# Performance work log

Hardware: AMD Instinct MI355X
Metric: run time of the kernel (lower is better)

Reference implementation:

```python
import jax, jax.numpy as jnp
import numpy as np

GH, GW, H, B, IN = 4, 2, 512, 8192, 1
FC_HID = H // 2
NC = GH * GW
BN_EPS = 1e-5


def setup_inputs() -> dict:
    key = jax.random.key(0)
    ks = jax.random.split(key, 20)
    def n(k, shape, s=1.0):
        return jax.random.normal(k, shape, dtype=jnp.float32) * s
    return {
        "x": n(ks[0], (B, GH, GW)),
        "h_ext": n(ks[1], (B, H), 0.1),
        "c_ext": n(ks[2], (B, H), 0.1),
        "grid_h": n(ks[3], (GH, GW, B, H), 0.1),
        "grid_c": n(ks[4], (GH, GW, B, H), 0.1),
        "Wh": n(ks[5], (NC, H, 3 * H), (3 * H) ** -0.5),
        "bh": n(ks[6], (NC, H), 0.01),
        "Wc": n(ks[7], (NC, H, 3 * H), (3 * H) ** -0.5),
        "bc": n(ks[8], (NC, H), 0.01),
        "W_ih": n(ks[9], (NC, 4 * H, IN), 1.0),
        "W_hh": n(ks[10], (NC, 4 * H, H), H ** -0.5),
        "b_ih": n(ks[11], (NC, 4 * H), 0.01),
        "b_hh": n(ks[12], (NC, 4 * H), 0.01),
        "W1": n(ks[13], (FC_HID, 2 * H), (2 * H) ** -0.5),
        "b1": n(ks[14], (FC_HID,), 0.01),
        "W2": n(ks[15], (1, FC_HID), FC_HID ** -0.5),
        "b2": n(ks[16], (1,), 0.01),
        "gamma": jnp.ones((1,), jnp.float32),
        "beta": jnp.zeros((1,), jnp.float32),
    }


def _lattice_forward(x, h_ext, c_ext, grid_h, grid_c, Wh, bh, Wc, bc,
                     W_ih, W_hh, b_ih, b_hh, W1, b1, W2, b2, gamma, beta):
    b = x.shape[0]
    zeros = jnp.zeros((b, H), x.dtype)
    # python lists over the small fixed 4x2 grid (strict left/up dependency)
    sh = [[grid_h[i, j] for j in range(GW)] for i in range(GH)]
    sc = [[grid_c[i, j] for j in range(GW)] for i in range(GH)]
    for i in range(GH):
        for j in range(GW):
            k = i * GW + j
            h_prev, c_prev = sh[i][j], sc[i][j]
            if i == 0 and j == 0:
                h_left, c_left = h_ext, c_ext
            elif j > 0:
                h_left, c_left = sh[i][j - 1], sc[i][j - 1]
            else:
                h_left, c_left = zeros, zeros
            if i > 0:
                h_up, c_up = sh[i - 1][j], sc[i - 1][j]
            else:
                h_up, c_up = zeros, zeros
            comb_h = jnp.concatenate([h_left, h_up, h_prev], axis=1)  # [B,3H]
            comb_c = jnp.concatenate([c_left, c_up, c_prev], axis=1)
            ph = comb_h @ Wh[k].T + bh[k]  # [B,H]
            pc = comb_c @ Wc[k].T + bc[k]
            xi = x[:, i, j][:, None]  # [B,1]
            gates = xi @ W_ih[k].T + b_ih[k] + ph @ W_hh[k].T + b_hh[k]  # [B,4H]
            ig, fg, gg, og = jnp.split(gates, 4, axis=1)
            c_new = jax.nn.sigmoid(fg) * pc + jax.nn.sigmoid(ig) * jnp.tanh(gg)
            h_new = jax.nn.sigmoid(og) * jnp.tanh(c_new)
            sh[i][j], sc[i][j] = h_new, c_new
    final_h = sh[-1][-1] + h_ext
    final_c = sc[-1][-1] + c_ext
    final = jnp.concatenate([final_h, final_c], axis=1)  # [B,2H]
    hid = jax.nn.relu(final @ W1.T + b1)
    out = hid @ W2.T + b2  # [B,1]
    # BatchNorm1d in training mode: biased batch stats over the batch dim
    mu = jnp.mean(out, axis=0, keepdims=True)
    var = jnp.mean((out - mu) ** 2, axis=0, keepdims=True)
    out = gamma * (out - mu) * jax.lax.rsqrt(var + BN_EPS) + beta
    out = jax.nn.sigmoid(out)
    new_gh = jnp.stack([jnp.stack(row) for row in sh])  # [GH,GW,B,H]
    new_gc = jnp.stack([jnp.stack(row) for row in sc])
    return out, final_h, final_c, new_gh, new_gc


def reference(x, h_ext, c_ext, grid_h, grid_c, Wh, bh, Wc, bc,
              W_ih, W_hh, b_ih, b_hh, W1, b1, W2, b2, gamma, beta):
    return _lattice_forward(x, h_ext, c_ext, grid_h, grid_c, Wh, bh, Wc, bc,
                            W_ih, W_hh, b_ih, b_hh, W1, b1, W2, b2, gamma, beta)
```

## Files before the change

kernel.cpp:

```cpp
#include <hip/hip_runtime.h>
#include <stdint.h>

#define B_SZ 8192
static const size_t BH = (size_t)B_SZ * 512;

typedef short bfrag8 __attribute__((ext_vector_type(8)));
typedef float f32x4 __attribute__((ext_vector_type(4)));

__device__ __forceinline__ unsigned short f2bf(float f) {
  union { float f; uint32_t u; } c; c.f = f;
  uint32_t u = c.u;
  uint32_t r = (u + 0x7FFFu + ((u >> 16) & 1u)) >> 16;
  return (unsigned short)r;
}
__device__ __forceinline__ float bf2f(unsigned short u) {
  union { uint32_t u; float f; } c; c.u = ((uint32_t)u) << 16;
  return c.f;
}
__device__ __forceinline__ uint32_t pk2(float a, float b) {
  uint32_t r;
  asm("v_cvt_pk_bf16_f32 %0, %1, %2" : "=v"(r) : "v"(a), "v"(b));
  return r;
}
__device__ __forceinline__ float sigm(float x) { return 1.0f / (1.0f + __expf(-x)); }
__device__ __forceinline__ float tanh_fast(float x) {
  float cx = fminf(fmaxf(x, -15.0f), 15.0f);
  float e = __expf(2.0f * cx);
  return (e - 1.0f) / (e + 1.0f);
}

__device__ __forceinline__ void gload16(const void* g, void* l) {
  __builtin_amdgcn_global_load_lds(
      (const __attribute__((address_space(1))) void*)g,
      (__attribute__((address_space(3))) void*)l, 16, 0, 0);
}

__device__ __forceinline__ void xcd_swizzle(int& bx, int& by, int& bz) {
  int nx = gridDim.x, ny = gridDim.y, nz = gridDim.z;
  int nwg = nx * ny * nz;
  int id = blockIdx.x + nx * (blockIdx.y + ny * blockIdx.z);
  int q = nwg >> 3, r = nwg & 7;
  int xcd = id & 7, lin = id >> 3;
  int swz = (xcd < r ? xcd * (q + 1) : r * (q + 1) + (xcd - r) * q) + lin;
  bx = swz % nx; swz /= nx;
  by = swz % ny; bz = swz / ny;
}

struct PJob {
  const void* A[3];
  int co[3];
  int nseg, relu;
  const unsigned short* B;
  const float* bias;
  unsigned short* outBf;
};
struct PArgs {
  PJob j[8];
  int ldA, ldB, outStride;
};

template <int AF32>
__global__ __launch_bounds__(256, 4) void pgemm_k(PArgs pa) {
  __shared__ __align__(16) char As[16384];
  __shared__ __align__(16) char Bs[16384];
  int bx, by, bz;
  xcd_swizzle(bx, by, bz);
  const PJob jb = pa.j[bz];
  const int tid = threadIdx.x;
  const int lane = tid & 63;
  const int wv = tid >> 6;
  const int wr = wv >> 1, wc = wv & 1;
  const int m0 = by * 128;
  const int ldA = pa.ldA;

  int rowA[4], cg[4];
  const char* browPtr[4];
#pragma unroll
  for (int q = 0; q < 4; ++q) {
    int cl = q * 256 + tid;
    int row = cl >> 3, cs = cl & 7;
    cg[q] = cs ^ (row & 7);
    rowA[q] = row;
    browPtr[q] = (const char*)jb.B + (size_t)(bx * 128 + row) * pa.ldB * 2;
  }

  f32x4 acc[4][4];
#pragma unroll
  for (int a = 0; a < 4; ++a)
#pragma unroll
    for (int b = 0; b < 4; ++b) acc[a][b] = f32x4{0.f, 0.f, 0.f, 0.f};

  for (int s = 0; s < jb.nseg; ++s) {
    const int coB = jb.co[s] * 2;
    for (int k0 = 0; k0 < 512; k0 += 64) {
#pragma unroll
      for (int q = 0; q < 4; ++q)
        gload16(browPtr[q] + coB + k0 * 2 + cg[q] * 16,
                Bs + (q * 256 + tid) * 16);
      if (AF32) {
        const float* Ab = (const float*)jb.A[s];
#pragma unroll
        for (int q = 0; q < 4; ++q) {
          const float4* p = (const float4*)(Ab + (size_t)(m0 + rowA[q]) * ldA +
                                            k0 + cg[q] * 8);
          float4 a0 = p[0];
          float4 a1 = p[1];
          uint4 w;
          w.x = pk2(a0.x, a0.y);
          w.y = pk2(a0.z, a0.w);
          w.z = pk2(a1.x, a1.y);
          w.w = pk2(a1.z, a1.w);
          *(uint4*)(As + (q * 256 + tid) * 16) = w;
        }
      } else {
        const char* Ab = (const char*)jb.A[s];
#pragma unroll
        for (int q = 0; q < 4; ++q)
          gload16(Ab + ((size_t)(m0 + rowA[q]) * ldA + k0) * 2 + cg[q] * 16,
                  As + (q * 256 + tid) * 16);
      }
      __syncthreads();
#pragma unroll
      for (int ks = 0; ks < 2; ++ks) {
        bfrag8 af[4], bfr[4];
#pragma unroll
        for (int mf = 0; mf < 4; ++mf) {
          int row = wr * 64 + mf * 16 + (lane & 15);
          af[mf] = *(const bfrag8*)(As + row * 128 +
                                    ((ks * 4 + (lane >> 4)) ^ (row & 7)) * 16);
        }
#pragma unroll
        for (int nf = 0; nf < 4; ++nf) {
          int row = wc * 64 + nf * 16 + (lane & 15);
          bfr[nf] = *(const bfrag8*)(Bs + row * 128 +
                                     ((ks * 4 + (lane >> 4)) ^ (row & 7)) * 16);
        }
#pragma unroll
        for (int mf = 0; mf < 4; ++mf)
#pragma unroll
          for (int nf = 0; nf < 4; ++nf)
            acc[mf][nf] = __builtin_amdgcn_mfma_f32_16x16x32_bf16(
                af[mf], bfr[nf], acc[mf][nf], 0, 0, 0);
      }
      __syncthreads();
    }
  }

  const int c4 = lane & 15;
  const int r4 = lane >> 4;
  const int n0 = bx * 128;
#pragma unroll
  for (int nf = 0; nf < 4; ++nf) {
    int colg = n0 + wc * 64 + nf * 16 + c4;
    float bv = jb.bias[colg];
#pragma unroll
    for (int mf = 0; mf < 4; ++mf)
#pragma unroll
      for (int r = 0; r < 4; ++r) {
        int rowg = m0 + wr * 64 + mf * 16 + r4 * 4 + r;
        size_t o = (size_t)rowg * pa.outStride + colg;
        float v = acc[mf][nf][r] + bv;
        if (jb.relu) v = fmaxf(v, 0.0f);
        jb.outBf[o] = f2bf(v);
      }
  }
}

struct GJob {
  const unsigned short* ph;
  const unsigned short* Whh;
  const unsigned short* pc;
  float* gh; float* gc;
  int cell, last;
};
struct GArgs {
  GJob j[2];
  const float* x;
  const float* W_ih; const float* b_ih; const float* b_hh;
  const float* h_ext; const float* c_ext;
  float* fh; float* fc;
  unsigned short* finalB;
};

__global__ __launch_bounds__(512, 2) void gates_k(GArgs ga) {
  extern __shared__ char lds[];
  int bx, by, bz;
  xcd_swizzle(bx, by, bz);
  const GJob jb = ga.j[bz];
  const int tid = threadIdx.x;
  const int lane = tid & 63;
  const int wv = tid >> 6;
  const int wr = wv >> 2;
  const int wc = wv & 3;
  const int m0 = by * 256;

  int rowS[4], cgS[4];
  const char* bPtr[4];
#pragma unroll
  for (int q = 0; q < 4; ++q) {
    int cl = q * 512 + tid;
    int row = cl >> 3, cs = cl & 7;
    cgS[q] = cs ^ (row & 7);
    rowS[q] = row;
    int browG = ((row >> 4) & 3) * 512 + bx * 64 + ((row >> 6) << 4) + (row & 15);
    bPtr[q] = (const char*)jb.Whh + (size_t)browG * 512 * 2;
  }

  auto stage = [&](int t, int buf) {
    int k0 = t << 6;
    char* Ab = lds + buf * 32768;
    char* Bb = lds + 65536 + buf * 32768;
#pragma unroll
    for (int q = 0; q < 4; ++q)
      gload16((const char*)jb.ph + ((size_t)(m0 + rowS[q]) * 512 + k0) * 2 + cgS[q] * 16,
              Ab + (q * 512 + tid) * 16);
#pragma unroll
    for (int q = 0; q < 4; ++q)
      gload16(bPtr[q] + k0 * 2 + cgS[q] * 16, Bb + (q * 512 + tid) * 16);
  };

  f32x4 acc[8][4];
#pragma unroll
  for (int a = 0; a < 8; ++a)
#pragma unroll
    for (int b = 0; b < 4; ++b) acc[a][b] = f32x4{0.f, 0.f, 0.f, 0.f};

  stage(0, 0);
  asm volatile("s_waitcnt vmcnt(0)" ::: "memory");
  __builtin_amdgcn_s_barrier();
  asm volatile("" ::: "memory");

  int cur = 0;
  for (int t = 0; t < 8; ++t) {
    if (t + 1 < 8) stage(t + 1, cur ^ 1);
    const char* As = lds + cur * 32768;
    const char* Bs = lds + 65536 + cur * 32768;
    bfrag8 bfr[4][2];
#pragma unroll
    for (int nf = 0; nf < 4; ++nf)
#pragma unroll
      for (int ks = 0; ks < 2; ++ks) {
        int row = wc * 64 + nf * 16 + (lane & 15);
        bfr[nf][ks] = *(const bfrag8*)(Bs + row * 128 +
                                       (((ks * 4 + (lane >> 4)) ^ (row & 7)) * 16));
      }
#pragma unroll
    for (int mf = 0; mf < 8; ++mf) {
      bfrag8 af[2];
#pragma unroll
      for (int ks = 0; ks < 2; ++ks) {
        int row = wr * 128 + mf * 16 + (lane & 15);
        af[ks] = *(const bfrag8*)(As + row * 128 +
                                  (((ks * 4 + (lane >> 4)) ^ (row & 7)) * 16));
      }
#pragma unroll
      for (int nf = 0; nf < 4; ++nf)
#pragma unroll
        for (int ks = 0; ks < 2; ++ks)
          acc[mf][nf] = __builtin_amdgcn_mfma_f32_16x16x32_bf16(
              af[ks], bfr[nf][ks], acc[mf][nf], 0, 0, 0);
    }
    asm volatile("s_waitcnt vmcnt(0)" ::: "memory");
    __builtin_amdgcn_s_barrier();
    asm volatile("" ::: "memory");
    cur ^= 1;
  }

  const int c4 = lane & 15;
  const int r4 = lane >> 4;
  int hcol = bx * 64 + wc * 16 + c4;
  const float* Wih = ga.W_ih + jb.cell * 2048;
  const float* bih = ga.b_ih + jb.cell * 2048;
  const float* bhh = ga.b_hh + jb.cell * 2048;
  float wih[4], gb[4];
#pragma unroll
  for (int q = 0; q < 4; ++q) {
    wih[q] = Wih[q * 512 + hcol];
    gb[q] = bih[q * 512 + hcol] + bhh[q * 512 + hcol];
  }
#pragma unroll
  for (int mf = 0; mf < 8; ++mf)
#pragma unroll
    for (int r = 0; r < 4; ++r) {
      int b = m0 + wr * 128 + mf * 16 + r4 * 4 + r;
      float xi = ga.x[b * 8 + jb.cell];
      float vi = acc[mf][0][r] + xi * wih[0] + gb[0];
      float vf = acc[mf][1][r] + xi * wih[1] + gb[1];
      float vg = acc[mf][2][r] + xi * wih[2] + gb[2];
      float vo = acc[mf][3][r] + xi * wih[3] + gb[3];
      size_t o = (size_t)b * 512 + hcol;
      float pcv = bf2f(jb.pc[o]);
      float cn = sigm(vf) * pcv + sigm(vi) * tanh_fast(vg);
      float hn = sigm(vo) * tanh_fast(cn);
      jb.gh[o] = hn;
      jb.gc[o] = cn;
      if (jb.last) {
        float fh = hn + ga.h_ext[o];
        float fc = cn + ga.c_ext[o];
        ga.fh[o] = fh;
        ga.fc[o] = fc;
        ga.finalB[(size_t)b * 1024 + hcol] = f2bf(fh);
        ga.finalB[(size_t)b * 1024 + 512 + hcol] = f2bf(fc);
      }
    }
}

struct CvtArgs {
  const float4* s[8];
  uint2* d[8];
  long start[9];
};
__global__ __launch_bounds__(256) void convert_many(CvtArgs ca) {
  long total = ca.start[8];
  long stride = (long)gridDim.x * blockDim.x;
  for (long idx = (long)blockIdx.x * blockDim.x + threadIdx.x; idx < total;
       idx += stride) {
    int jb = 0;
#pragma unroll
    for (int q = 1; q < 8; ++q) jb += (idx >= ca.start[q]) ? 1 : 0;
    long local = idx - ca.start[jb];
    float4 v = ca.s[jb][local];
    uint2 o;
    o.x = (uint32_t)f2bf(v.x) | ((uint32_t)f2bf(v.y) << 16);
    o.y = (uint32_t)f2bf(v.z) | ((uint32_t)f2bf(v.w) << 16);
    ca.d[jb][local] = o;
  }
}

__global__ __launch_bounds__(256)
void fc2_kernel(const unsigned short* hid, const float* W2, const float* b2,
                float* outlin) {
  int row = blockIdx.x * 4 + (threadIdx.x >> 6);
  int lane = threadIdx.x & 63;
  uint2 hv = ((const uint2*)(hid + (size_t)row * 256))[lane];
  float4 wv = ((const float4*)W2)[lane];
  float s = bf2f((unsigned short)(hv.x & 0xffffu)) * wv.x +
            bf2f((unsigned short)(hv.x >> 16)) * wv.y +
            bf2f((unsigned short)(hv.y & 0xffffu)) * wv.z +
            bf2f((unsigned short)(hv.y >> 16)) * wv.w;
#pragma unroll
  for (int o = 32; o > 0; o >>= 1) s += __shfl_down(s, o);
  if (lane == 0) outlin[row] = s + b2[0];
}

__global__ __launch_bounds__(1024)
void bn_kernel(const float* outlin, const float* gamma, const float* beta,
               float* out) {
  __shared__ float sred[16], sred2[16];
  __shared__ float smu, srs;
  float s = 0.f, s2 = 0.f;
  for (int i = threadIdx.x; i < 8192; i += 1024) {
    float v = outlin[i];
    s += v; s2 += v * v;
  }
#pragma unroll
  for (int o = 32; o > 0; o >>= 1) { s += __shfl_down(s, o); s2 += __shfl_down(s2, o); }
  if ((threadIdx.x & 63) == 0) { sred[threadIdx.x >> 6] = s; sred2[threadIdx.x >> 6] = s2; }
  __syncthreads();
  if (threadIdx.x == 0) {
    float S = 0.f, S2 = 0.f;
    for (int q = 0; q < 16; ++q) { S += sred[q]; S2 += sred2[q]; }
    float mu = S * (1.0f / 8192.0f);
    float var = S2 * (1.0f / 8192.0f) - mu * mu;
    smu = mu; srs = rsqrtf(var + 1e-5f);
  }
  __syncthreads();
  float gm = gamma[0], bt = beta[0];
  for (int i = threadIdx.x; i < 8192; i += 1024) {
    float v = (outlin[i] - smu) * srs * gm + bt;
    out[i] = sigm(v);
  }
}

extern "C" void kernel_launch(void* const* d_in, const int* in_sizes, int n_in,
                              void* d_out, int out_size, void* d_ws, size_t ws_size,
                              hipStream_t stream) {
  const float* x      = (const float*)d_in[0];
  const float* h_ext  = (const float*)d_in[1];
  const float* c_ext  = (const float*)d_in[2];
  const float* grid_h = (const float*)d_in[3];
  const float* grid_c = (const float*)d_in[4];
  const float* Wh     = (const float*)d_in[5];
  const float* bh     = (const float*)d_in[6];
  const float* Wc     = (const float*)d_in[7];
  const float* bc     = (const float*)d_in[8];
  const float* W_ih   = (const float*)d_in[9];
  const float* W_hh   = (const float*)d_in[10];
  const float* b_ih   = (const float*)d_in[11];
  const float* b_hh   = (const float*)d_in[12];
  const float* W1     = (const float*)d_in[13];
  const float* b1     = (const float*)d_in[14];
  const float* W2     = (const float*)d_in[15];
  const float* b2     = (const float*)d_in[16];
  const float* gamma  = (const float*)d_in[17];
  const float* beta   = (const float*)d_in[18];

  float* out = (float*)d_out;
  float* fh_out = out + 8192;
  float* fc_out = fh_out + BH;
  float* gh_out = fc_out + BH;
  float* gc_out = gh_out + 8 * BH;

  char* ws = (char*)d_ws;
  size_t off = 0;
  auto alloc = [&](size_t bytes) {
    char* p = ws + off;
    off = (off + bytes + 255) & ~(size_t)255;
    return p;
  };
  unsigned short* whB   = (unsigned short*)alloc(8ull * 512 * 1536 * 2);
  unsigned short* wcB   = (unsigned short*)alloc(8ull * 512 * 1536 * 2);
  unsigned short* whhB  = (unsigned short*)alloc(8ull * 2048 * 512 * 2);
  unsigned short* w1B   = (unsigned short*)alloc(256ull * 1024 * 2);
  unsigned short* pcB   = (unsigned short*)alloc(8 * BH * 2);
  unsigned short* phB   = (unsigned short*)alloc(8 * BH * 2);
  unsigned short* finalB = (unsigned short*)alloc((size_t)B_SZ * 1024 * 2);
  unsigned short* hidB   = (unsigned short*)alloc((size_t)B_SZ * 256 * 2);
  float*          outlin = (float*)alloc((size_t)B_SZ * 4);

  hipFuncSetAttribute((const void*)gates_k,
                      hipFuncAttributeMaxDynamicSharedMemorySize, 131072);

  {
    CvtArgs ca;
    long n4[4] = {8L * 512 * 1536 / 4, 8L * 512 * 1536 / 4,
                  8L * 2048 * 512 / 4, 256L * 1024 / 4};
    const float* srcs[4] = {Wh, Wc, W_hh, W1};
    unsigned short* dsts[4] = {whB, wcB, whhB, w1B};
    ca.start[0] = 0;
    for (int q = 0; q < 8; ++q) {
      int qq = q < 4 ? q : 3;
      ca.s[q] = (const float4*)srcs[qq];
      ca.d[q] = (uint2*)dsts[qq];
      ca.start[q + 1] = ca.start[q] + (q < 4 ? n4[q] : 0);
    }
    convert_many<<<2048, 256, 0, stream>>>(ca);
  }

  auto launch_p = [&](const int* cells, int n) {
    PArgs pa = {};
    pa.ldA = 512; pa.ldB = 1536; pa.outStride = 512;
    for (int q = 0; q < n; ++q) {
      int k = cells[q];
      int i = k >> 1, jj = k & 1;
      PJob& jh = pa.j[2 * q];
      PJob& jc = pa.j[2 * q + 1];
      jh = PJob{}; jc = PJob{};
      int ns = 0;
      if (k == 0) {
        jh.A[ns] = h_ext; jc.A[ns] = c_ext;
        jh.co[ns] = 0; jc.co[ns] = 0; ns++;
      } else if (jj > 0) {
        jh.A[ns] = gh_out + (size_t)(k - 1) * BH;
        jc.A[ns] = gc_out + (size_t)(k - 1) * BH;
        jh.co[ns] = 0; jc.co[ns] = 0; ns++;
      }
      if (i > 0) {
        jh.A[ns] = gh_out + (size_t)(k - 2) * BH;
        jc.A[ns] = gc_out + (size_t)(k - 2) * BH;
        jh.co[ns] = 512; jc.co[ns] = 512; ns++;
      }
      jh.A[ns] = grid_h + (size_t)k * BH;
      jc.A[ns] = grid_c + (size_t)k * BH;
      jh.co[ns] = 1024; jc.co[ns] = 1024; ns++;
      jh.nseg = ns; jc.nseg = ns;
      jh.B = whB + (size_t)k * 512 * 1536; jh.bias = bh + k * 512;
      jc.B = wcB + (size_t)k * 512 * 1536; jc.bias = bc + k * 512;
      jh.outBf = phB + (size_t)k * BH;
      jc.outBf = pcB + (size_t)k * BH;
    }
    pgemm_k<1><<<dim3(4, 64, 2 * n), 256, 0, stream>>>(pa);
  };

  auto launch_gates = [&](const int* cells, int n) {
    GArgs ga = {};
    ga.x = x; ga.W_ih = W_ih; ga.b_ih = b_ih; ga.b_hh = b_hh;
    ga.h_ext = h_ext; ga.c_ext = c_ext;
    ga.fh = fh_out; ga.fc = fc_out; ga.finalB = finalB;
    for (int q = 0; q < n; ++q) {
      int k = cells[q];
      GJob& j = ga.j[q];
      j.ph = phB + (size_t)k * BH;
      j.Whh = whhB + (size_t)k * 2048 * 512;
      j.pc = pcB + (size_t)k * BH;
      j.gh = gh_out + (size_t)k * BH;
      j.gc = gc_out + (size_t)k * BH;
      j.cell = k; j.last = (k == 7);
    }
    gates_k<<<dim3(8, 32, n), 512, 131072, stream>>>(ga);
  };

  const int diags[5][2] = {{0, -1}, {1, 2}, {3, 4}, {5, 6}, {7, -1}};
  const int dn[5] = {1, 2, 2, 2, 1};
  for (int d = 0; d < 5; ++d) {
    launch_p(diags[d], dn[d]);
    launch_gates(diags[d], dn[d]);
  }

  {
    PArgs pa = {};
    pa.ldA = 1024; pa.ldB = 1024; pa.outStride = 256;
    PJob& j = pa.j[0];
    j = PJob{};
    j.A[0] = finalB; j.co[0] = 0;
    j.A[1] = finalB + 512; j.co[1] = 512;
    j.nseg = 2; j.relu = 1;
    j.B = w1B; j.bias = b1; j.outBf = hidB;
    pgemm_k<0><<<dim3(2, 64, 1), 256, 0, stream>>>(pa);
  }

  fc2_kernel<<<2048, 256, 0, stream>>>(hidB, W2, b2, outlin);
  bn_kernel<<<1, 1024, 0, stream>>>(outlin, gamma, beta, out);
}
```

Measured before the change: 732.9 us.

## Use 256x256 double-buffered GEMM tile kernel for lattice projection GEMMs

Replaces the 128x128 single-buffered projection GEMM with a new 256x256-tile, 512-thread kernel that double-buffers A and B in 128KB dynamic LDS. The next tile's fp32 A loads and B global-to-LDS copies are issued before the MFMAs on the current tile, and the bf16 conversion of A is written afterwards. The larger tile cuts global reloads per output and hides load latency. In exchange occupancy drops to one block per CU, fewer blocks launch per diagonal, and register pressure rises with 32 accumulators. The old kernel is kept, without its fp32 path, for the FC1 GEMM.

New measurement: 663.6 us. 9.5% less time.

```diff
diff --git a/kernel.cpp b/kernel.cpp
--- a/kernel.cpp
+++ b/kernel.cpp
@@ -46,122 +46,142 @@
   by = swz % ny; bz = swz / ny;
 }
 
-struct PJob {
-  const void* A[3];
+struct P8Job {
+  const float* A[3];
   int co[3];
-  int nseg, relu;
+  int nseg;
   const unsigned short* B;
   const float* bias;
   unsigned short* outBf;
 };
-struct PArgs {
-  PJob j[8];
-  int ldA, ldB, outStride;
+struct P8Args {
+  P8Job j[4];
+  int ldB, outStride;
 };
 
-template <int AF32>
-__global__ __launch_bounds__(256, 4) void pgemm_k(PArgs pa) {
-  __shared__ __align__(16) char As[16384];
-  __shared__ __align__(16) char Bs[16384];
+__global__ __launch_bounds__(512, 1) void pgemm256_k(P8Args pa) {
+  extern __shared__ char lds[];
   int bx, by, bz;
   xcd_swizzle(bx, by, bz);
-  const PJob jb = pa.j[bz];
+  const P8Job jb = pa.j[bz];
   const int tid = threadIdx.x;
   const int lane = tid & 63;
   const int wv = tid >> 6;
-  const int wr = wv >> 1, wc = wv & 1;
-  const int m0 = by * 128;
-  const int ldA = pa.ldA;
-
-  int rowA[4], cg[4];
-  const char* browPtr[4];
+  const int wr = wv >> 2, wc = wv & 3;
+  const int m0 = by * 256;
+
+  int rowS[4], cgS[4];
+  const char* bPtr[4];
 #pragma unroll
   for (int q = 0; q < 4; ++q) {
-    int cl = q * 256 + tid;
+    int cl = q * 512 + tid;
     int row = cl >> 3, cs = cl & 7;
-    cg[q] = cs ^ (row & 7);
-    rowA[q] = row;
-    browPtr[q] = (const char*)jb.B + (size_t)(bx * 128 + row) * pa.ldB * 2;
-  }
-
-  f32x4 acc[4][4];
-#pragma unroll
-  for (int a = 0; a < 4; ++a)
+    cgS[q] = cs ^ (row & 7);
+    rowS[q] = row;
+    bPtr[q] = (const char*)jb.B + (size_t)(bx * 256 + row) * pa.ldB * 2;
+  }
+
+  auto loadA = [&](int t, float4* a0, float4* a1) {
+    int seg = t >> 3, k0 = (t & 7) << 6;
+    const float* Ab = jb.A[seg];
+#pragma unroll
+    for (int q = 0; q < 4; ++q) {
+      const float4* p = (const float4*)(Ab + (size_t)(m0 + rowS[q]) * 512 + k0 +
+                                        cgS[q] * 8);
+      a0[q] = p[0];
+      a1[q] = p[1];
+    }
+  };
+  auto stageB = [&](int t, int buf) {
+    int seg = t >> 3, k0 = (t & 7) << 6;
+    int coB = (jb.co[seg] + k0) * 2;
+    char* Bb = lds + 65536 + buf * 32768;
+#pragma unroll
+    for (int q = 0; q < 4; ++q)
+      gload16(bPtr[q] + coB + cgS[q] * 16, Bb + (q * 512 + tid) * 16);
+  };
+  auto writeA = [&](const float4* a0, const float4* a1, int buf) {
+    char* Ab = lds + buf * 32768;
+#pragma unroll
+    for (int q = 0; q < 4; ++q) {
+      uint4 w;
+      w.x = pk2(a0[q].x, a0[q].y);
+      w.y = pk2(a0[q].z, a0[q].w);
+      w.z = pk2(a1[q].x, a1[q].y);
+      w.w = pk2(a1[q].z, a1[q].w);
+      *(uint4*)(Ab + (q * 512 + tid) * 16) = w;
+    }
+  };
+
+  f32x4 acc[8][4];
+#pragma unroll
+  for (int a = 0; a < 8; ++a)
 #pragma unroll
     for (int b = 0; b < 4; ++b) acc[a][b] = f32x4{0.f, 0.f, 0.f, 0.f};
 
-  for (int s = 0; s < jb.nseg; ++s) {
-    const int coB = jb.co[s] * 2;
-    for (int k0 = 0; k0 < 512; k0 += 64) {
-#pragma unroll
-      for (int q = 0; q < 4; ++q)
-        gload16(browPtr[q] + coB + k0 * 2 + cg[q] * 16,
-                Bs + (q * 256 + tid) * 16);
-      if (AF32) {
-        const float* Ab = (const float*)jb.A[s];
-#pragma unroll
-        for (int q = 0; q < 4; ++q) {
-          const float4* p = (const float4*)(Ab + (size_t)(m0 + rowA[q]) * ldA +
-                                            k0 + cg[q] * 8);
-          float4 a0 = p[0];
-          float4 a1 = p[1];
-          uint4 w;
-          w.x = pk2(a0.x, a0.y);
-          w.y = pk2(a0.z, a0.w);
-          w.z = pk2(a1.x, a1.y);
-          w.w = pk2(a1.z, a1.w);
-          *(uint4*)(As + (q * 256 + tid) * 16) = w;
-        }
-      } else {
-        const char* Ab = (const char*)jb.A[s];
-#pragma unroll
-        for (int q = 0; q < 4; ++q)
-          gload16(Ab + ((size_t)(m0 + rowA[q]) * ldA + k0) * 2 + cg[q] * 16,
-                  As + (q * 256 + tid) * 16);
-      }
-      __syncthreads();
+  const int nt = jb.nseg * 8;
+
+  {
+    float4 a0[4], a1[4];
+    loadA(0, a0, a1);
+    stageB(0, 0);
+    writeA(a0, a1, 0);
+  }
+  __syncthreads();
+
+  int cur = 0;
+  for (int t = 0; t < nt; ++t) {
+    float4 a0[4], a1[4];
+    const bool more = (t + 1 < nt);
+    if (more) {
+      loadA(t + 1, a0, a1);
+      stageB(t + 1, cur ^ 1);
+    }
+    const char* As = lds + cur * 32768;
+    const char* Bs = lds + 65536 + cur * 32768;
+    bfrag8 bfr[4][2];
+#pragma unroll
+    for (int nf = 0; nf < 4; ++nf)
 #pragma unroll
       for (int ks = 0; ks < 2; ++ks) {
-        bfrag8 af[4], bfr[4];
-#pragma unroll
-        for (int mf = 0; mf < 4; ++mf) {
-          int row = wr * 64 + mf * 16 + (lane & 15);
-          af[mf] = *(const bfrag8*)(As + row * 128 +
-                                    ((ks * 4 + (lane >> 4)) ^ (row & 7)) * 16);
-        }
-#pragma unroll
-        for (int nf = 0; nf < 4; ++nf) {
-          int row = wc * 64 + nf * 16 + (lane & 15);
-          bfr[nf] = *(const bfrag8*)(Bs + row * 128 +
-                                     ((ks * 4 + (lane >> 4)) ^ (row & 7)) * 16);
-        }
-#pragma unroll
-        for (int mf = 0; mf < 4; ++mf)
-#pragma unroll
-          for (int nf = 0; nf < 4; ++nf)
-            acc[mf][nf] = __builtin_amdgcn_mfma_f32_16x16x32_bf16(
-                af[mf], bfr[nf], acc[mf][nf], 0, 0, 0);
-      }
-      __syncthreads();
-    }
+        int row = wc * 64 + nf * 16 + (lane & 15);
+        bfr[nf][ks] = *(const bfrag8*)(Bs + row * 128 +
+                                       (((ks * 4 + (lane >> 4)) ^ (row & 7)) * 16));
+      }
+#pragma unroll
+    for (int mf = 0; mf < 8; ++mf) {
+      bfrag8 af[2];
+#pragma unroll
+      for (int ks = 0; ks < 2; ++ks) {
+        int row = wr * 128 + mf * 16 + (lane & 15);
+        af[ks] = *(const bfrag8*)(As + row * 128 +
+                                  (((ks * 4 + (lane >> 4)) ^ (row & 7)) * 16));
+      }
+#pragma unroll
+      for (int nf = 0; nf < 4; ++nf)
+#pragma unroll
+        for (int ks = 0; ks < 2; ++ks)
+          acc[mf][nf] = __builtin_amdgcn_mfma_f32_16x16x32_bf16(
+              af[ks], bfr[nf][ks], acc[mf][nf], 0, 0, 0);
+    }
+    if (more) writeA(a0, a1, cur ^ 1);
+    __syncthreads();
+    cur ^= 1;
   }
 
   const int c4 = lane & 15;
   const int r4 = lane >> 4;
-  const int n0 = bx * 128;
+  const int n0 = bx * 256;
 #pragma unroll
   for (int nf = 0; nf < 4; ++nf) {
     int colg = n0 + wc * 64 + nf * 16 + c4;
     float bv = jb.bias[colg];
 #pragma unroll
-    for (int mf = 0; mf < 4; ++mf)
+    for (int mf = 0; mf < 8; ++mf)
 #pragma unroll
       for (int r = 0; r < 4; ++r) {
-        int rowg = m0 + wr * 64 + mf * 16 + r4 * 4 + r;
-        size_t o = (size_t)rowg * pa.outStride + colg;
-        float v = acc[mf][nf][r] + bv;
-        if (jb.relu) v = fmaxf(v, 0.0f);
-        jb.outBf[o] = f2bf(v);
+        int rowg = m0 + wr * 128 + mf * 16 + r4 * 4 + r;
+        jb.outBf[(size_t)rowg * pa.outStride + colg] = f2bf(acc[mf][nf][r] + bv);
       }
   }
 }
@@ -303,6 +323,107 @@
         ga.finalB[(size_t)b * 1024 + 512 + hcol] = f2bf(fc);
       }
     }
+}
+
+struct PJob {
+  const void* A[3];
+  int co[3];
+  int nseg, relu;
+  const unsigned short* B;
+  const float* bias;
+  unsigned short* outBf;
+};
+struct PArgs {
+  PJob j[8];
+  int ldA, ldB, outStride;
+};
+
+__global__ __launch_bounds__(256, 4) void pgemm_k(PArgs pa) {
+  __shared__ __align__(16) char As[16384];
+  __shared__ __align__(16) char Bs[16384];
+  int bx, by, bz;
+  xcd_swizzle(bx, by, bz);
+  const PJob jb = pa.j[bz];
+  const int tid = threadIdx.x;
+  const int lane = tid & 63;
+  const int wv = tid >> 6;
+  const int wr = wv >> 1, wc = wv & 1;
+  const int m0 = by * 128;
+
+  int rowA[4], cg[4];
+  const char* browPtr[4];
+#pragma unroll
+  for (int q = 0; q < 4; ++q) {
+    int cl = q * 256 + tid;
+    int row = cl >> 3, cs = cl & 7;
+    cg[q] = cs ^ (row & 7);
+    rowA[q] = row;
+    browPtr[q] = (const char*)jb.B + (size_t)(bx * 128 + row) * pa.ldB * 2;
+  }
+
+  f32x4 acc[4][4];
+#pragma unroll
+  for (int a = 0; a < 4; ++a)
+#pragma unroll
+    for (int b = 0; b < 4; ++b) acc[a][b] = f32x4{0.f, 0.f, 0.f, 0.f};
+
+  for (int s = 0; s < jb.nseg; ++s) {
+    const char* Abase = (const char*)jb.A[s];
+    const int coB = jb.co[s] * 2;
+    for (int k0 = 0; k0 < 512; k0 += 64) {
+#pragma unroll
+      for (int q = 0; q < 4; ++q)
+        gload16(Abase + ((size_t)(m0 + rowA[q]) * pa.ldA + k0) * 2 + cg[q] * 16,
+                As + (q * 256 + tid) * 16);
+#pragma unroll
+      for (int q = 0; q < 4; ++q)
+        gload16(browPtr[q] + coB + k0 * 2 + cg[q] * 16,
+                Bs + (q * 256 + tid) * 16);
+      __syncthreads();
+#pragma unroll
+      for (int ks = 0; ks < 2; ++ks) {
+        bfrag8 af[4], bfr[4];
+#pragma unroll
+        for (int mf = 0; mf < 4; ++mf) {
+          int row = wr * 64 + mf * 16 + (lane & 15);
+          af[mf] = *(const bfrag8*)(As + row * 128 +
+                                    ((ks * 4 + (lane >> 4)) ^ (row & 7)) * 16);
+        }
+#pragma unroll
+        for (int nf = 0; nf < 4; ++nf) {
+          int row = wc * 64 + nf * 16 + (lane & 15);
+          bfr[nf] = *(const bfrag8*)(Bs + row * 128 +
+                                     ((ks * 4 + (lane >> 4)) ^ (row & 7)) * 16);
+        }
+#pragma unroll
+        for (int mf = 0; mf < 4; ++mf)
+#pragma unroll
+          for (int nf = 0; nf < 4; ++nf)
+            acc[mf][nf] = __builtin_amdgcn_mfma_f32_16x16x32_bf16(
+                af[mf], bfr[nf], acc[mf][nf], 0, 0, 0);
+      }
+      __syncthreads();
+    }
+  }
+
+  const int c4 = lane & 15;
+  const int r4 = lane >> 4;
+  const int n0 = bx * 128;
+#pragma unroll
+  for (int nf = 0; nf < 4; ++nf) {
+    int colg = n0 + wc * 64 + nf * 16 + c4;
+    float bv = jb.bias[colg];
+#pragma unroll
+    for (int mf = 0; mf < 4; ++mf)
+#pragma unroll
+      for (int r = 0; r < 4; ++r) {
+        int rowg = m0 + wr * 64 + mf * 16 + r4 * 4 + r;
+        size_t o = (size_t)rowg * pa.outStride + colg;
+        float v = acc[mf][nf][r] + bv;
+        if (jb.relu) v = fmaxf(v, 0.0f);
+        jb.outBf[o] = f2bf(v);
+      }
+  }
 }
 
 struct CvtArgs {
@@ -420,6 +541,8 @@
 
   hipFuncSetAttribute((const void*)gates_k,
                       hipFuncAttributeMaxDynamicSharedMemorySize, 131072);
+  hipFuncSetAttribute((const void*)pgemm256_k,
+                      hipFuncAttributeMaxDynamicSharedMemorySize, 131072);
 
   {
     CvtArgs ca;
@@ -438,14 +561,14 @@
   }
 
   auto launch_p = [&](const int* cells, int n) {
-    PArgs pa = {};
-    pa.ldA = 512; pa.ldB = 1536; pa.outStride = 512;
+    P8Args pa = {};
+    pa.ldB = 1536; pa.outStride = 512;
     for (int q = 0; q < n; ++q) {
       int k = cells[q];
       int i = k >> 1, jj = k & 1;
-      PJob& jh = pa.j[2 * q];
-      PJob& jc = pa.j[2 * q + 1];
-      jh = PJob{}; jc = PJob{};
+      P8Job& jh = pa.j[2 * q];
+      P8Job& jc = pa.j[2 * q + 1];
+      jh = P8Job{}; jc = P8Job{};
       int ns = 0;
       if (k == 0) {
         jh.A[ns] = h_ext; jc.A[ns] = c_ext;
@@ -469,7 +592,7 @@
       jh.outBf = phB + (size_t)k * BH;
       jc.outBf = pcB + (size_t)k * BH;
     }
-    pgemm_k<1><<<dim3(4, 64, 2 * n), 256, 0, stream>>>(pa);
+    pgemm256_k<<<dim3(2, 32, 2 * n), 512, 131072, stream>>>(pa);
   };
 
   auto launch_gates = [&](const int* cells, int n) {
@@ -506,7 +629,7 @@
     j.A[1] = finalB + 512; j.co[1] = 512;
     j.nseg = 2; j.relu = 1;
     j.B = w1B; j.bias = b1; j.outBf = hidB;
-    pgemm_k<0><<<dim3(2, 64, 1), 256, 0, stream>>>(pa);
+    pgemm_k<<<dim3(2, 64, 1), 256, 0, stream>>>(pa);
   }
 
   fc2_kernel<<<2048, 256, 0, stream>>>(hidB, W2, b2, outlin);
```
